# Performance work log

Hardware: AMD Instinct MI355X
Metric: run time of the kernel (lower is better)

The kernel has to match this reference:

```python
import jax, jax.numpy as jnp
import numpy as np

B, L, V, D = 8, 1024, 64, 64  # num_vars == d_model required by the module's g*h broadcast
EPS = 1e-5


def _layer_norm(x, gamma, beta):
    mu = jnp.mean(x, axis=-1, keepdims=True)
    var = jnp.mean(jnp.square(x - mu), axis=-1, keepdims=True)
    return (x - mu) * jax.lax.rsqrt(var + EPS) * gamma + beta


def setup_inputs() -> dict:
    key = jax.random.key(0)
    ks = jax.random.split(key, 20)
    s = 0.05
    inp = {
        'x': jax.random.normal(ks[0], (B, L, V), jnp.float32),
        # per-variable GRN(1, D, D) params, batched over V
        'W1': jax.random.normal(ks[1], (V, D), jnp.float32) * s,   # lin1 weight [in=1 -> D]
        'b1': jax.random.normal(ks[2], (V, D), jnp.float32) * s,
        'W2': jax.random.normal(ks[3], (V, D, D), jnp.float32) * s,
        'b2': jax.random.normal(ks[4], (V, D), jnp.float32) * s,
        'Wg': jax.random.normal(ks[5], (V, D, D), jnp.float32) * s,
        'bg': jax.random.normal(ks[6], (V, D), jnp.float32) * s,
        'Wsk': jax.random.normal(ks[7], (V, D), jnp.float32) * s,  # skip Linear(1, D)
        'bsk': jax.random.normal(ks[8], (V, D), jnp.float32) * s,
        'gamma': jnp.ones((V, D), jnp.float32),
        'beta': jnp.zeros((V, D), jnp.float32),
        # weight_net GRN(V*D, D, V) params
        'Wn1': jax.random.normal(ks[9], (V * D, D), jnp.float32) * s,
        'bn1': jax.random.normal(ks[10], (D,), jnp.float32) * s,
        'Wn2': jax.random.normal(ks[11], (D, D), jnp.float32) * s,
        'bn2': jax.random.normal(ks[12], (D,), jnp.float32) * s,
        'Wng': jax.random.normal(ks[13], (D, V), jnp.float32) * s,
        'bng': jax.random.normal(ks[14], (V,), jnp.float32) * s,
        'Wns': jax.random.normal(ks[15], (V * D, V), jnp.float32) * s,
        'bns': jax.random.normal(ks[16], (V,), jnp.float32) * s,
        'ngamma': jnp.ones((V,), jnp.float32),
        'nbeta': jnp.zeros((V,), jnp.float32),
    }
    return inp


def reference(x, W1, b1, W2, b2, Wg, bg, Wsk, bsk, gamma, beta,
              Wn1, bn1, Wn2, bn2, Wng, bng, Wns, bns, ngamma, nbeta):
    Bx, Lx, Vx = x.shape
    # --- per-variable GRN(1, D, D), batched over the variable axis ---
    h1 = jax.nn.elu(x[..., None] * W1 + b1)                      # [B,L,V,D]
    h2 = jnp.einsum('blvd,vde->blve', h1, W2) + b2               # [B,L,V,D]
    g = jax.nn.sigmoid(jnp.einsum('blvd,vde->blve', h2, Wg) + bg)
    skip = x[..., None] * Wsk + bsk                              # [B,L,V,D]
    stacked = _layer_norm(skip + g * h2, gamma, beta)            # [B,L,V,D]
    # --- weight net GRN(V*D, D, V) + softmax (note: requires V == D) ---
    flat = stacked.reshape(Bx, Lx, Vx * stacked.shape[-1])
    hw = jax.nn.elu(flat @ Wn1 + bn1)                            # [B,L,D]
    hw = hw @ Wn2 + bn2                                          # [B,L,D]
    gw = jax.nn.sigmoid(hw @ Wng + bng)                          # [B,L,V]
    skw = flat @ Wns + bns                                       # [B,L,V]
    weights = jax.nn.softmax(_layer_norm(skw + gw * hw, ngamma, nbeta), axis=-1)
    return jnp.einsum('blv,blvd->bld', weights, stacked)
```

## Files before the change

kernel.cpp:

```cpp
#include <hip/hip_runtime.h>
#include <hip/hip_bf16.h>
#include <math.h>

#define NV 64
#define ND 64
#define NTOK 8192
#define LN_EPS 1e-5f
#define KSPLIT 8
#define KRANGE (4096 / KSPLIT)
#define SROW 4160
#define WROW 4160
#define PROW 1056

typedef __attribute__((ext_vector_type(8))) short s8v;
typedef __attribute__((ext_vector_type(4))) float f4v;
typedef __attribute__((ext_vector_type(4))) int   i4v;

__device__ __forceinline__ float sigm_f(float x) { return 1.f / (1.f + __expf(-x)); }
__device__ __forceinline__ float elu_f(float x)  { return x > 0.f ? x : (__expf(x) - 1.f); }

__device__ __forceinline__ float bf16_to_f(unsigned short s) {
    union { unsigned int u; float f; } c; c.u = ((unsigned int)s) << 16;
    return c.f;
}
__device__ __forceinline__ unsigned short bf16_rn(float f) {
    union { float f; unsigned int u; } c; c.f = f;
    return (unsigned short)((c.u + 0x8000u) >> 16);
}

__global__ __launch_bounds__(256) void vsn_prepack(
    const float* __restrict__ W2, const float* __restrict__ Wg,
    const float* __restrict__ Wn1, const float* __restrict__ Wns,
    short* __restrict__ w2b, short* __restrict__ wgb,
    short* __restrict__ wct)
{
    __shared__ float T[64][65];
    const int b = blockIdx.x, t = threadIdx.x;

    if (b < 64) {
        const float* src = W2 + (size_t)b * 4096;
        short* dst = w2b + (size_t)b * 4096;
        #pragma unroll
        for (int pass = 0; pass < 2; ++pass) {
            #pragma unroll
            for (int i = 0; i < 16; ++i) {
                int id = i * 256 + t;
                T[id & 63][id >> 6] = src[id];
            }
            __syncthreads();
            #pragma unroll
            for (int i = 0; i < 16; ++i) {
                int id = i * 256 + t;
                dst[id] = (short)bf16_rn(T[id >> 6][id & 63]);
            }
            __syncthreads();
            src = Wg + (size_t)b * 4096;
            dst = wgb + (size_t)b * 4096;
        }
    } else {
        int tb = b - 64;
        int half = tb >> 6, kt = tb & 63;
        const float* src = (half == 0 ? Wn1 : Wns) + (size_t)(kt * 64) * 64;
        #pragma unroll
        for (int i = 0; i < 16; ++i) {
            int id = i * 256 + t;
            T[id & 63][id >> 6] = src[id];
        }
        __syncthreads();
        #pragma unroll
        for (int i = 0; i < 16; ++i) {
            int id = i * 256 + t;
            int n = id >> 6, r = id & 63;
            wct[(size_t)(half * 64 + n) * WROW + kt * 64 + r] = (short)bf16_rn(T[n][r]);
        }
    }
}

__global__ __launch_bounds__(256) void vsn_stage1(
    const float* __restrict__ x,
    const float* __restrict__ W1, const float* __restrict__ b1,
    const short* __restrict__ w2b, const short* __restrict__ wgb,
    const float* __restrict__ b2, const float* __restrict__ bg,
    const float* __restrict__ Wsk, const float* __restrict__ bsk,
    const float* __restrict__ gamma, const float* __restrict__ beta,
    unsigned short* __restrict__ stb)
{
    const int t = threadIdx.x;
    const int wave = t >> 6, lane = t & 63;
    const int m16 = lane & 15, quad = lane >> 4;
    const int v = blockIdx.y * 4 + wave;

    __shared__ float xs[4][32];
    __shared__ __align__(16) unsigned short h2s[4][32][72];

    float w1k[2][8], b1k[2][8];
    #pragma unroll
    for (int kt = 0; kt < 2; ++kt) {
        *(float4*)&w1k[kt][0] = *(const float4*)(W1 + v * 64 + kt * 32 + quad * 8);
        *(float4*)&w1k[kt][4] = *(const float4*)(W1 + v * 64 + kt * 32 + quad * 8 + 4);
        *(float4*)&b1k[kt][0] = *(const float4*)(b1 + v * 64 + kt * 32 + quad * 8);
        *(float4*)&b1k[kt][4] = *(const float4*)(b1 + v * 64 + kt * 32 + quad * 8 + 4);
    }
    float b2d[4], bgd[4], wskd[4], bskd[4], gamd[4], betd[4];
    #pragma unroll
    for (int ni = 0; ni < 4; ++ni) {
        int d = v * 64 + ni * 16 + m16;
        b2d[ni] = b2[d]; bgd[ni] = bg[d]; wskd[ni] = Wsk[d]; bskd[ni] = bsk[d];
        gamd[ni] = gamma[d]; betd[ni] = beta[d];
    }
    const size_t wb = (size_t)v * 4096;

    for (int tt4 = 0; tt4 < 4; ++tt4) {
        const int tile0 = blockIdx.x * 128 + tt4 * 32;

        if (lane < 32) xs[wave][lane] = x[(size_t)(tile0 + lane) * NV + v];

        s8v a[2][2];
        #pragma unroll
        for (int kt = 0; kt < 2; ++kt)
            #pragma unroll
            for (int mi = 0; mi < 2; ++mi) {
                float xv = xs[wave][mi * 16 + m16];
                float h[8];
                #pragma unroll
                for (int j = 0; j < 8; ++j) h[j] = elu_f(fmaf(xv, w1k[kt][j], b1k[kt][j]));
                i4v av;
                #pragma unroll
                for (int p = 0; p < 4; ++p) {
                    unsigned int u0 = __float_as_uint(h[2 * p]);
                    unsigned int u1 = __float_as_uint(h[2 * p + 1]);
                    av[p] = (int)((u1 & 0xffff0000u) | (u0 >> 16));
                }
                a[mi][kt] = *(s8v*)&av;
            }

        f4v hacc[2][4];
        #pragma unroll
        for (int mi = 0; mi < 2; ++mi)
            #pragma unroll
            for (int ni = 0; ni < 4; ++ni) hacc[mi][ni] = (f4v){0.f, 0.f, 0.f, 0.f};
        #pragma unroll
        for (int ni = 0; ni < 4; ++ni)
            #pragma unroll
            for (int kt = 0; kt < 2; ++kt) {
                s8v bh = *(const s8v*)(w2b + wb + (size_t)(ni * 16 + m16) * 64 + kt * 32 + quad * 8);
                #pragma unroll
                for (int mi = 0; mi < 2; ++mi)
                    hacc[mi][ni] = __builtin_amdgcn_mfma_f32_16x16x32_bf16(a[mi][kt], bh, hacc[mi][ni], 0, 0, 0);
            }
        #pragma unroll
        for (int mi = 0; mi < 2; ++mi)
            #pragma unroll
            for (int ni = 0; ni < 4; ++ni)
                #pragma unroll
                for (int r = 0; r < 4; ++r) hacc[mi][ni][r] += b2d[ni];

        #pragma unroll
        for (int mi = 0; mi < 2; ++mi)
            #pragma unroll
            for (int ni = 0; ni < 4; ++ni)
                #pragma unroll
                for (int r = 0; r < 4; ++r)
                    h2s[wave][mi * 16 + quad * 4 + r][ni * 16 + m16] =
                        (unsigned short)(__float_as_uint(hacc[mi][ni][r]) >> 16);

        s8v c[2][2];
        #pragma unroll
        for (int mi = 0; mi < 2; ++mi)
            #pragma unroll
            for (int kt = 0; kt < 2; ++kt)
                c[mi][kt] = *(const s8v*)&h2s[wave][mi * 16 + m16][kt * 32 + quad * 8];

        f4v gacc[2][4];
        #pragma unroll
        for (int mi = 0; mi < 2; ++mi)
            #pragma unroll
            for (int ni = 0; ni < 4; ++ni) gacc[mi][ni] = (f4v){0.f, 0.f, 0.f, 0.f};
        #pragma unroll
        for (int ni = 0; ni < 4; ++ni)
            #pragma unroll
            for (int kt = 0; kt < 2; ++kt) {
                s8v bh = *(const s8v*)(wgb + wb + (size_t)(ni * 16 + m16) * 64 + kt * 32 + quad * 8);
                #pragma unroll
                for (int mi = 0; mi < 2; ++mi)
                    gacc[mi][ni] = __builtin_amdgcn_mfma_f32_16x16x32_bf16(c[mi][kt], bh, gacc[mi][ni], 0, 0, 0);
            }

        {
            float xtok[2][4];
            #pragma unroll
            for (int mi = 0; mi < 2; ++mi)
                #pragma unroll
                for (int r = 0; r < 4; ++r) xtok[mi][r] = xs[wave][mi * 16 + quad * 4 + r];
            #pragma unroll
            for (int mi = 0; mi < 2; ++mi)
                #pragma unroll
                for (int ni = 0; ni < 4; ++ni)
                    #pragma unroll
                    for (int r = 0; r < 4; ++r) {
                        float g = sigm_f(gacc[mi][ni][r] + bgd[ni]);
                        gacc[mi][ni][r] = fmaf(xtok[mi][r], wskd[ni], bskd[ni]) + g * hacc[mi][ni][r];
                    }
        }

        #pragma unroll
        for (int mi = 0; mi < 2; ++mi)
            #pragma unroll
            for (int r = 0; r < 4; ++r) {
                float s0 = gacc[mi][0][r], s1 = gacc[mi][1][r], s2 = gacc[mi][2][r], s3 = gacc[mi][3][r];
                float sum = s0 + s1 + s2 + s3;
                float sq  = s0 * s0 + s1 * s1 + s2 * s2 + s3 * s3;
                #pragma unroll
                for (int m = 1; m < 16; m <<= 1) { sum += __shfl_xor(sum, m); sq += __shfl_xor(sq, m); }
                float mu  = sum * 0.015625f;
                float var = sq * 0.015625f - mu * mu;
                float rs  = rsqrtf(var + LN_EPS);
                size_t base = (size_t)(tile0 + mi * 16 + quad * 4 + r) * SROW + (size_t)v * 64 + m16;
                #pragma unroll
                for (int ni = 0; ni < 4; ++ni)
                    stb[base + ni * 16] =
                        bf16_rn((gacc[mi][ni][r] - mu) * rs * gamd[ni] + betd[ni]);
            }
    }
}

__global__ __launch_bounds__(512) void vsn_stage2a(
    const unsigned short* __restrict__ stb,
    const short* __restrict__ wct,
    float* __restrict__ part)
{
    const int t = threadIdx.x;
    const int wave = t >> 6, lane = t & 63;
    const int mtile = wave >> 2;
    const int n0 = (wave & 3) * 32;
    const int tok0 = blockIdx.x * 128 + mtile * 64;
    const int s = blockIdx.y;
    const int k0 = s * KRANGE;
    const int m16 = lane & 15, quad = lane >> 4;

    const short* A = (const short*)stb;

    f4v acc[4][2];
    #pragma unroll
    for (int i = 0; i < 4; ++i)
        #pragma unroll
        for (int j = 0; j < 2; ++j)
            acc[i][j] = (f4v){0.f, 0.f, 0.f, 0.f};

    const short* arow = A   + (size_t)(tok0 + m16) * SROW + quad * 8;
    const short* brow = wct + (size_t)(n0 + m16) * WROW + quad * 8;

    for (int k = k0; k < k0 + KRANGE; k += 32) {
        s8v a[4], b[2];
        #pragma unroll
        for (int i = 0; i < 4; ++i)
            a[i] = *(const s8v*)(arow + (size_t)i * 16 * SROW + k);
        #pragma unroll
        for (int j = 0; j < 2; ++j)
            b[j] = *(const s8v*)(brow + (size_t)j * 16 * WROW + k);
        #pragma unroll
        for (int i = 0; i < 4; ++i)
            #pragma unroll
            for (int j = 0; j < 2; ++j)
                acc[i][j] = __builtin_amdgcn_mfma_f32_16x16x32_bf16(a[i], b[j], acc[i][j], 0, 0, 0);
    }

    #pragma unroll
    for (int i = 0; i < 4; ++i)
        #pragma unroll
        for (int j = 0; j < 2; ++j)
            #pragma unroll
            for (int r = 0; r < 4; ++r)
                part[(size_t)(tok0 + i * 16 + quad * 4 + r) * PROW
                     + s * 128 + n0 + j * 16 + m16] = acc[i][j][r];
}

__global__ __launch_bounds__(256) void vsn_stage2b(
    const unsigned short* __restrict__ stb, const float* __restrict__ part,
    const float* __restrict__ bn1,
    const float* __restrict__ Wn2, const float* __restrict__ bn2,
    const float* __restrict__ Wng, const float* __restrict__ bng,
    const float* __restrict__ bns,
    const float* __restrict__ ngamma, const float* __restrict__ nbeta,
    float* __restrict__ out)
{
    const int t = threadIdx.x;
    const int tok0 = blockIdx.x * 8;
    const int lane = t & 63, wv = t >> 6;

    __shared__ __align__(16) float hw1_s[8][64];
    __shared__ __align__(16) float skw_s[8][64];
    __shared__ __align__(16) float hw2_s[8][64];
    __shared__ float s2_s[8][64];
    __shared__ float w_s[8][64];

    #pragma unroll
    for (int tk = 0; tk < 2; ++tk) {
        int tl = wv * 2 + tk;
        const float* pr = part + (size_t)(tok0 + tl) * PROW
                        + (lane >> 5) * 128 + (lane & 31) * 4;
        float tv[4] = {0.f, 0.f, 0.f, 0.f};
        #pragma unroll
        for (int i = 0; i < 4; ++i) {
            float4 a = *(const float4*)(pr + i * 256);
            tv[0] += a.x; tv[1] += a.y; tv[2] += a.z; tv[3] += a.w;
        }
        #pragma unroll
        for (int c = 0; c < 4; ++c) tv[c] += __shfl_xor(tv[c], 32);
        if (lane < 16) {
            int j0 = lane * 4;
            float4 bb = *(const float4*)(bn1 + j0);
            hw1_s[tl][j0 + 0] = elu_f(tv[0] + bb.x);
            hw1_s[tl][j0 + 1] = elu_f(tv[1] + bb.y);
            hw1_s[tl][j0 + 2] = elu_f(tv[2] + bb.z);
            hw1_s[tl][j0 + 3] = elu_f(tv[3] + bb.w);
        } else if (lane < 32) {
            int j0 = (lane - 16) * 4;
            float4 bb = *(const float4*)(bns + j0);
            skw_s[tl][j0 + 0] = tv[0] + bb.x;
            skw_s[tl][j0 + 1] = tv[1] + bb.y;
            skw_s[tl][j0 + 2] = tv[2] + bb.z;
            skw_s[tl][j0 + 3] = tv[3] + bb.w;
        }
    }
    __syncthreads();

    #pragma unroll
    for (int i = 0; i < 2; ++i) {
        int oidx = i * 256 + t;
        int tt = oidx >> 6, jj = oidx & 63;
        float acc = bn2[jj];
        #pragma unroll
        for (int k4 = 0; k4 < 16; ++k4) {
            float4 h = *(const float4*)&hw1_s[tt][k4 * 4];
            acc += h.x * Wn2[(k4*4+0)*64+jj] + h.y * Wn2[(k4*4+1)*64+jj]
                 + h.z * Wn2[(k4*4+2)*64+jj] + h.w * Wn2[(k4*4+3)*64+jj];
        }
        hw2_s[tt][jj] = acc;
    }
    __syncthreads();

    #pragma unroll
    for (int i = 0; i < 2; ++i) {
        int oidx = i * 256 + t;
        int tt = oidx >> 6, vv = oidx & 63;
        float acc = bng[vv];
        #pragma unroll
        for (int k4 = 0; k4 < 16; ++k4) {
            float4 h = *(const float4*)&hw2_s[tt][k4 * 4];
            acc += h.x * Wng[(k4*4+0)*64+vv] + h.y * Wng[(k4*4+1)*64+vv]
                 + h.z * Wng[(k4*4+2)*64+vv] + h.w * Wng[(k4*4+3)*64+vv];
        }
        float gw = sigm_f(acc);
        s2_s[tt][vv] = skw_s[tt][vv] + gw * hw2_s[tt][vv];
    }
    __syncthreads();

    const int vloc = lane >> 3, d8 = (lane & 7) * 8;
    s8v r0[8], r1[8];
    {
        const short* s0 = (const short*)stb + (size_t)(tok0 + wv * 2) * SROW + d8;
        const short* s1 = s0 + SROW;
        #pragma unroll
        for (int vc = 0; vc < 8; ++vc) {
            r0[vc] = *(const s8v*)(s0 + (vc * 8 + vloc) * 64);
            r1[vc] = *(const s8v*)(s1 + (vc * 8 + vloc) * 64);
        }
    }

    if (t < 128) {
        int tt = t >> 4, l = t & 15;
        float z[4]; float sum = 0.f, sq = 0.f;
        #pragma unroll
        for (int i = 0; i < 4; ++i) { z[i] = s2_s[tt][l + 16 * i]; sum += z[i]; sq += z[i] * z[i]; }
        #pragma unroll
        for (int m = 1; m < 16; m <<= 1) { sum += __shfl_xor(sum, m); sq += __shfl_xor(sq, m); }
        float mu  = sum * 0.015625f;
        float var = sq * 0.015625f - mu * mu;
        float rs  = rsqrtf(var + LN_EPS);
        float ln[4]; float mx = -1e30f;
        #pragma unroll
        for (int i = 0; i < 4; ++i) {
            ln[i] = (z[i] - mu) * rs * ngamma[l + 16 * i] + nbeta[l + 16 * i];
            mx = fmaxf(mx, ln[i]);
        }
        #pragma unroll
        for (int m = 1; m < 16; m <<= 1) mx = fmaxf(mx, __shfl_xor(mx, m));
        float es = 0.f; float ev[4];
        #pragma unroll
        for (int i = 0; i < 4; ++i) { ev[i] = __expf(ln[i] - mx); es += ev[i]; }
        #pragma unroll
        for (int m = 1; m < 16; m <<= 1) es += __shfl_xor(es, m);
        float inv = 1.f / es;
        #pragma unroll
        for (int i = 0; i < 4; ++i) w_s[tt][l + 16 * i] = ev[i] * inv;
    }
    __syncthreads();

    {
        float acc0[8], acc1[8];
        #pragma unroll
        for (int j = 0; j < 8; ++j) { acc0[j] = 0.f; acc1[j] = 0.f; }
        #pragma unroll
        for (int vc = 0; vc < 8; ++vc) {
            int v = vc * 8 + vloc;
            float w0 = w_s[wv * 2][v], w1 = w_s[wv * 2 + 1][v];
            #pragma unroll
            for (int j = 0; j < 8; ++j) {
                acc0[j] = fmaf(w0, bf16_to_f((unsigned short)r0[vc][j]), acc0[j]);
                acc1[j] = fmaf(w1, bf16_to_f((unsigned short)r1[vc][j]), acc1[j]);
            }
        }
        #pragma unroll
        for (int m = 8; m <= 32; m <<= 1)
            #pragma unroll
            for (int j = 0; j < 8; ++j) {
                acc0[j] += __shfl_xor(acc0[j], m);
                acc1[j] += __shfl_xor(acc1[j], m);
            }
        if (lane < 8) {
            float* op = out + (size_t)(tok0 + wv * 2) * 64 + lane * 8;
            *(float4*)op       = make_float4(acc0[0], acc0[1], acc0[2], acc0[3]);
            *(float4*)(op + 4) = make_float4(acc0[4], acc0[5], acc0[6], acc0[7]);
            op += 64;
            *(float4*)op       = make_float4(acc1[0], acc1[1], acc1[2], acc1[3]);
            *(float4*)(op + 4) = make_float4(acc1[4], acc1[5], acc1[6], acc1[7]);
        }
    }
}

extern "C" void kernel_launch(void* const* d_in, const int* in_sizes, int n_in,
                              void* d_out, int out_size, void* d_ws, size_t ws_size,
                              hipStream_t stream) {
    const float* x     = (const float*)d_in[0];
    const float* W1    = (const float*)d_in[1];
    const float* b1    = (const float*)d_in[2];
    const float* W2    = (const float*)d_in[3];
    const float* b2    = (const float*)d_in[4];
    const float* Wg    = (const float*)d_in[5];
    const float* bg    = (const float*)d_in[6];
    const float* Wsk   = (const float*)d_in[7];
    const float* bsk   = (const float*)d_in[8];
    const float* gamma = (const float*)d_in[9];
    const float* beta  = (const float*)d_in[10];
    const float* Wn1   = (const float*)d_in[11];
    const float* bn1   = (const float*)d_in[12];
    const float* Wn2   = (const float*)d_in[13];
    const float* bn2   = (const float*)d_in[14];
    const float* Wng   = (const float*)d_in[15];
    const float* bng   = (const float*)d_in[16];
    const float* Wns   = (const float*)d_in[17];
    const float* bns   = (const float*)d_in[18];
    const float* ngam  = (const float*)d_in[19];
    const float* nbet  = (const float*)d_in[20];

    char* ws = (char*)d_ws;
    unsigned short* stb = (unsigned short*)ws;
    short* wct = (short*)(ws + (70u << 20));
    float* part = (float*)(ws + (72u << 20));
    short* w2b = (short*)(ws + (108u << 20));
    short* wgb = w2b + 262144;
    float* outp = (float*)d_out;

    vsn_prepack<<<dim3(192), 256, 0, stream>>>(W2, Wg, Wn1, Wns, w2b, wgb, wct);
    vsn_stage1<<<dim3(NTOK / 128, 16), 256, 0, stream>>>(
        x, W1, b1, w2b, wgb, b2, bg, Wsk, bsk, gamma, beta, stb);
    vsn_stage2a<<<dim3(NTOK / 128, KSPLIT), 512, 0, stream>>>(stb, wct, part);
    vsn_stage2b<<<dim3(NTOK / 8), 256, 0, stream>>>(
        stb, part, bn1, Wn2, bn2, Wng, bng, bns, ngam, nbet, outp);
}
```

Baseline: 222.8 us.

## Fuse split-K weight-net GEMM into epilogue kernel with in-LDS reduction

Merges the split-K GEMM kernel and the weight-net epilogue kernel into one 1024-thread kernel handling 32 tokens per block. The four K-quarters are reduced through shared memory instead of a global partial-sum buffer. This removes the global write and read of partials and one launch. In exchange, per-block tiles are smaller, so each block rereads the full Wn1/Wns weight matrix for only 32 tokens. The large LDS footprint also limits occupancy.

```diff
diff --git a/kernel.cpp b/kernel.cpp
--- a/kernel.cpp
+++ b/kernel.cpp
@@ -6,11 +6,8 @@
 #define ND 64
 #define NTOK 8192
 #define LN_EPS 1e-5f
-#define KSPLIT 8
-#define KRANGE (4096 / KSPLIT)
 #define SROW 4160
 #define WROW 4160
-#define PROW 1056
 
 typedef __attribute__((ext_vector_type(8))) short s8v;
 typedef __attribute__((ext_vector_type(4))) float f4v;
@@ -224,59 +221,9 @@
     }
 }
 
-__global__ __launch_bounds__(512) void vsn_stage2a(
+__global__ __launch_bounds__(1024) void vsn_stage2(
     const unsigned short* __restrict__ stb,
     const short* __restrict__ wct,
-    float* __restrict__ part)
-{
-    const int t = threadIdx.x;
-    const int wave = t >> 6, lane = t & 63;
-    const int mtile = wave >> 2;
-    const int n0 = (wave & 3) * 32;
-    const int tok0 = blockIdx.x * 128 + mtile * 64;
-    const int s = blockIdx.y;
-    const int k0 = s * KRANGE;
-    const int m16 = lane & 15, quad = lane >> 4;
-
-    const short* A = (const short*)stb;
-
-    f4v acc[4][2];
-    #pragma unroll
-    for (int i = 0; i < 4; ++i)
-        #pragma unroll
-        for (int j = 0; j < 2; ++j)
-            acc[i][j] = (f4v){0.f, 0.f, 0.f, 0.f};
-
-    const short* arow = A   + (size_t)(tok0 + m16) * SROW + quad * 8;
-    const short* brow = wct + (size_t)(n0 + m16) * WROW + quad * 8;
-
-    for (int k = k0; k < k0 + KRANGE; k += 32) {
-        s8v a[4], b[2];
-        #pragma unroll
-        for (int i = 0; i < 4; ++i)
-            a[i] = *(const s8v*)(arow + (size_t)i * 16 * SROW + k);
-        #pragma unroll
-        for (int j = 0; j < 2; ++j)
-            b[j] = *(const s8v*)(brow + (size_t)j * 16 * WROW + k);
-        #pragma unroll
-        for (int i = 0; i < 4; ++i)
-            #pragma unroll
-            for (int j = 0; j < 2; ++j)
-                acc[i][j] = __builtin_amdgcn_mfma_f32_16x16x32_bf16(a[i], b[j], acc[i][j], 0, 0, 0);
-    }
-
-    #pragma unroll
-    for (int i = 0; i < 4; ++i)
-        #pragma unroll
-        for (int j = 0; j < 2; ++j)
-            #pragma unroll
-            for (int r = 0; r < 4; ++r)
-                part[(size_t)(tok0 + i * 16 + quad * 4 + r) * PROW
-                     + s * 128 + n0 + j * 16 + m16] = acc[i][j][r];
-}
-
-__global__ __launch_bounds__(256) void vsn_stage2b(
-    const unsigned short* __restrict__ stb, const float* __restrict__ part,
     const float* __restrict__ bn1,
     const float* __restrict__ Wn2, const float* __restrict__ bn2,
     const float* __restrict__ Wng, const float* __restrict__ bng,
@@ -285,81 +232,107 @@
     float* __restrict__ out)
 {
     const int t = threadIdx.x;
-    const int tok0 = blockIdx.x * 8;
-    const int lane = t & 63, wv = t >> 6;
-
-    __shared__ __align__(16) float hw1_s[8][64];
-    __shared__ __align__(16) float skw_s[8][64];
-    __shared__ __align__(16) float hw2_s[8][64];
-    __shared__ float s2_s[8][64];
-    __shared__ float w_s[8][64];
-
-    #pragma unroll
-    for (int tk = 0; tk < 2; ++tk) {
-        int tl = wv * 2 + tk;
-        const float* pr = part + (size_t)(tok0 + tl) * PROW
-                        + (lane >> 5) * 128 + (lane & 31) * 4;
-        float tv[4] = {0.f, 0.f, 0.f, 0.f};
-        #pragma unroll
-        for (int i = 0; i < 4; ++i) {
-            float4 a = *(const float4*)(pr + i * 256);
-            tv[0] += a.x; tv[1] += a.y; tv[2] += a.z; tv[3] += a.w;
-        }
-        #pragma unroll
-        for (int c = 0; c < 4; ++c) tv[c] += __shfl_xor(tv[c], 32);
-        if (lane < 16) {
-            int j0 = lane * 4;
-            float4 bb = *(const float4*)(bn1 + j0);
-            hw1_s[tl][j0 + 0] = elu_f(tv[0] + bb.x);
-            hw1_s[tl][j0 + 1] = elu_f(tv[1] + bb.y);
-            hw1_s[tl][j0 + 2] = elu_f(tv[2] + bb.z);
-            hw1_s[tl][j0 + 3] = elu_f(tv[3] + bb.w);
-        } else if (lane < 32) {
-            int j0 = (lane - 16) * 4;
-            float4 bb = *(const float4*)(bns + j0);
-            skw_s[tl][j0 + 0] = tv[0] + bb.x;
-            skw_s[tl][j0 + 1] = tv[1] + bb.y;
-            skw_s[tl][j0 + 2] = tv[2] + bb.z;
-            skw_s[tl][j0 + 3] = tv[3] + bb.w;
-        }
+    const int wave = t >> 6, lane = t & 63;
+    const int m16 = lane & 15, quad = lane >> 4;
+    const int kq = wave >> 2;
+    const int mtile = wave & 1, nh = (wave >> 1) & 1;
+    const int tok0 = blockIdx.x * 32;
+
+    __shared__ __align__(16) float P[3][32][132];
+    float (*S)[132] = P[0];
+    float* base1 = &P[1][0][0];
+    float (*hw1)[64] = (float(*)[64])base1;
+    float (*skw)[64] = (float(*)[64])(base1 + 2048);
+    float (*hw2)[64] = (float(*)[64])(&P[2][0][0]);
+    float (*s2m)[64] = hw1;
+    float (*wgt)[64] = skw;
+
+    const short* A = (const short*)stb;
+    const int k0 = kq * 1024;
+
+    f4v acc[4];
+    #pragma unroll
+    for (int nj = 0; nj < 4; ++nj) acc[nj] = (f4v){0.f, 0.f, 0.f, 0.f};
+
+    const short* arow = A + (size_t)(tok0 + mtile * 16 + m16) * SROW + k0 + quad * 8;
+    const short* brow = wct + (size_t)(nh * 64 + m16) * WROW + k0 + quad * 8;
+
+    #pragma unroll 4
+    for (int kk = 0; kk < 1024; kk += 32) {
+        s8v a0 = *(const s8v*)(arow + kk);
+        s8v b[4];
+        #pragma unroll
+        for (int nj = 0; nj < 4; ++nj)
+            b[nj] = *(const s8v*)(brow + (size_t)nj * 16 * WROW + kk);
+        #pragma unroll
+        for (int nj = 0; nj < 4; ++nj)
+            acc[nj] = __builtin_amdgcn_mfma_f32_16x16x32_bf16(a0, b[nj], acc[nj], 0, 0, 0);
+    }
+
+    if (kq >= 1) {
+        #pragma unroll
+        for (int nj = 0; nj < 4; ++nj)
+            #pragma unroll
+            for (int r = 0; r < 4; ++r)
+                P[kq - 1][mtile * 16 + quad * 4 + r][nh * 64 + nj * 16 + m16] = acc[nj][r];
+    }
+    __syncthreads();
+    if (kq == 0) {
+        #pragma unroll
+        for (int nj = 0; nj < 4; ++nj)
+            #pragma unroll
+            for (int r = 0; r < 4; ++r) {
+                int row = mtile * 16 + quad * 4 + r, col = nh * 64 + nj * 16 + m16;
+                float v = acc[nj][r] + P[0][row][col] + P[1][row][col] + P[2][row][col];
+                S[row][col] = v;
+            }
     }
     __syncthreads();
 
     #pragma unroll
     for (int i = 0; i < 2; ++i) {
-        int oidx = i * 256 + t;
-        int tt = oidx >> 6, jj = oidx & 63;
-        float acc = bn2[jj];
+        int idx = i * 1024 + t;
+        int m = idx >> 6, j = idx & 63;
+        hw1[m][j] = elu_f(S[m][j] + bn1[j]);
+        skw[m][j] = S[m][64 + j] + bns[j];
+    }
+    __syncthreads();
+
+    #pragma unroll
+    for (int i = 0; i < 2; ++i) {
+        int idx = i * 1024 + t;
+        int m = idx >> 6, j = idx & 63;
+        float a2 = bn2[j];
         #pragma unroll
         for (int k4 = 0; k4 < 16; ++k4) {
-            float4 h = *(const float4*)&hw1_s[tt][k4 * 4];
-            acc += h.x * Wn2[(k4*4+0)*64+jj] + h.y * Wn2[(k4*4+1)*64+jj]
-                 + h.z * Wn2[(k4*4+2)*64+jj] + h.w * Wn2[(k4*4+3)*64+jj];
-        }
-        hw2_s[tt][jj] = acc;
+            float4 h = *(const float4*)&hw1[m][k4 * 4];
+            a2 += h.x * Wn2[(k4*4+0)*64+j] + h.y * Wn2[(k4*4+1)*64+j]
+                + h.z * Wn2[(k4*4+2)*64+j] + h.w * Wn2[(k4*4+3)*64+j];
+        }
+        hw2[m][j] = a2;
     }
     __syncthreads();
 
     #pragma unroll
     for (int i = 0; i < 2; ++i) {
-        int oidx = i * 256 + t;
-        int tt = oidx >> 6, vv = oidx & 63;
-        float acc = bng[vv];
+        int idx = i * 1024 + t;
+        int m = idx >> 6, vv = idx & 63;
+        float a3 = bng[vv];
         #pragma unroll
         for (int k4 = 0; k4 < 16; ++k4) {
-            float4 h = *(const float4*)&hw2_s[tt][k4 * 4];
-            acc += h.x * Wng[(k4*4+0)*64+vv] + h.y * Wng[(k4*4+1)*64+vv]
-                 + h.z * Wng[(k4*4+2)*64+vv] + h.w * Wng[(k4*4+3)*64+vv];
-        }
-        float gw = sigm_f(acc);
-        s2_s[tt][vv] = skw_s[tt][vv] + gw * hw2_s[tt][vv];
+            float4 h = *(const float4*)&hw2[m][k4 * 4];
+            a3 += h.x * Wng[(k4*4+0)*64+vv] + h.y * Wng[(k4*4+1)*64+vv]
+                + h.z * Wng[(k4*4+2)*64+vv] + h.w * Wng[(k4*4+3)*64+vv];
+        }
+        float gw = sigm_f(a3);
+        s2m[m][vv] = skw[m][vv] + gw * hw2[m][vv];
     }
     __syncthreads();
 
     const int vloc = lane >> 3, d8 = (lane & 7) * 8;
     s8v r0[8], r1[8];
     {
-        const short* s0 = (const short*)stb + (size_t)(tok0 + wv * 2) * SROW + d8;
+        const short* s0 = A + (size_t)(tok0 + wave * 2) * SROW + d8;
         const short* s1 = s0 + SROW;
         #pragma unroll
         for (int vc = 0; vc < 8; ++vc) {
@@ -368,11 +341,11 @@
         }
     }
 
-    if (t < 128) {
+    if (t < 512) {
         int tt = t >> 4, l = t & 15;
         float z[4]; float sum = 0.f, sq = 0.f;
         #pragma unroll
-        for (int i = 0; i < 4; ++i) { z[i] = s2_s[tt][l + 16 * i]; sum += z[i]; sq += z[i] * z[i]; }
+        for (int i = 0; i < 4; ++i) { z[i] = s2m[tt][l + 16 * i]; sum += z[i]; sq += z[i] * z[i]; }
         #pragma unroll
         for (int m = 1; m < 16; m <<= 1) { sum += __shfl_xor(sum, m); sq += __shfl_xor(sq, m); }
         float mu  = sum * 0.015625f;
@@ -393,7 +366,7 @@
         for (int m = 1; m < 16; m <<= 1) es += __shfl_xor(es, m);
         float inv = 1.f / es;
         #pragma unroll
-        for (int i = 0; i < 4; ++i) w_s[tt][l + 16 * i] = ev[i] * inv;
+        for (int i = 0; i < 4; ++i) wgt[tt][l + 16 * i] = ev[i] * inv;
     }
     __syncthreads();
 
@@ -404,7 +377,7 @@
         #pragma unroll
         for (int vc = 0; vc < 8; ++vc) {
             int v = vc * 8 + vloc;
-            float w0 = w_s[wv * 2][v], w1 = w_s[wv * 2 + 1][v];
+            float w0 = wgt[wave * 2][v], w1 = wgt[wave * 2 + 1][v];
             #pragma unroll
             for (int j = 0; j < 8; ++j) {
                 acc0[j] = fmaf(w0, bf16_to_f((unsigned short)r0[vc][j]), acc0[j]);
@@ -419,7 +392,7 @@
                 acc1[j] += __shfl_xor(acc1[j], m);
             }
         if (lane < 8) {
-            float* op = out + (size_t)(tok0 + wv * 2) * 64 + lane * 8;
+            float* op = out + (size_t)(tok0 + wave * 2) * 64 + lane * 8;
             *(float4*)op       = make_float4(acc0[0], acc0[1], acc0[2], acc0[3]);
             *(float4*)(op + 4) = make_float4(acc0[4], acc0[5], acc0[6], acc0[7]);
             op += 64;
@@ -457,15 +430,13 @@
     char* ws = (char*)d_ws;
     unsigned short* stb = (unsigned short*)ws;
     short* wct = (short*)(ws + (70u << 20));
-    float* part = (float*)(ws + (72u << 20));
-    short* w2b = (short*)(ws + (108u << 20));
+    short* w2b = (short*)(ws + (72u << 20));
     short* wgb = w2b + 262144;
     float* outp = (float*)d_out;
 
     vsn_prepack<<<dim3(192), 256, 0, stream>>>(W2, Wg, Wn1, Wns, w2b, wgb, wct);
     vsn_stage1<<<dim3(NTOK / 128, 16), 256, 0, stream>>>(
         x, W1, b1, w2b, wgb, b2, bg, Wsk, bsk, gamma, beta, stb);
-    vsn_stage2a<<<dim3(NTOK / 128, KSPLIT), 512, 0, stream>>>(stb, wct, part);
-    vsn_stage2b<<<dim3(NTOK / 8), 256, 0, stream>>>(
-        stb, part, bn1, Wn2, bn2, Wng, bng, bns, ngam, nbet, outp);
-}
+    vsn_stage2<<<dim3(NTOK / 32), 1024, 0, stream>>>(
+        stb, wct, bn1, Wn2, bn2, Wng, bng, bns, ngam, nbet, outp);
+}
```

After: 240.6 us. 1.08x slower.

## Stage weight-net GEMM tiles through LDS with register prefetch and finer K-split

Applied to the files above, without the earlier changes.

Rewrites the split-K GEMM of flattened stacked activations against the weight-net matrices so each 256-thread block stages 128x64 bf16 tiles of A and B into padded shared memory. It prefetches the next K chunk into registers while computing on the current one. Each wave now computes a 32x128 output tile, so B fragments are reused from LDS instead of being reloaded from global memory. The K split doubles to 16, which doubles the partial-sum buffer that stage2b must reduce. Row strides drop their padding (4160 to 4096), which may reintroduce cache-set conflicts on global loads, and the workspace layout is compacted.

```diff
diff --git a/kernel.cpp b/kernel.cpp
--- a/kernel.cpp
+++ b/kernel.cpp
@@ -6,11 +6,12 @@
 #define ND 64
 #define NTOK 8192
 #define LN_EPS 1e-5f
-#define KSPLIT 8
-#define KRANGE (4096 / KSPLIT)
-#define SROW 4160
-#define WROW 4160
-#define PROW 1056
+#define SROW 4096
+#define WROW 4096
+#define KSPLIT 16
+#define KR2 (4096 / KSPLIT)
+#define BK 64
+#define PROW2 (KSPLIT * 128)
 
 typedef __attribute__((ext_vector_type(8))) short s8v;
 typedef __attribute__((ext_vector_type(4))) float f4v;
@@ -224,55 +225,81 @@
     }
 }
 
-__global__ __launch_bounds__(512) void vsn_stage2a(
+__global__ __launch_bounds__(256) void vsn_stage2a(
     const unsigned short* __restrict__ stb,
     const short* __restrict__ wct,
     float* __restrict__ part)
 {
     const int t = threadIdx.x;
     const int wave = t >> 6, lane = t & 63;
-    const int mtile = wave >> 2;
-    const int n0 = (wave & 3) * 32;
-    const int tok0 = blockIdx.x * 128 + mtile * 64;
+    const int m16 = lane & 15, quad = lane >> 4;
+    const int tok0 = blockIdx.x * 128;
     const int s = blockIdx.y;
-    const int k0 = s * KRANGE;
-    const int m16 = lane & 15, quad = lane >> 4;
-
+    const int k0 = s * KR2;
+
+    __shared__ __align__(16) unsigned short Al[128][72];
+    __shared__ __align__(16) unsigned short Bl[128][72];
+
+    const int srow = t >> 3;
+    const int scol = (t & 7) * 8;
     const short* A = (const short*)stb;
 
-    f4v acc[4][2];
-    #pragma unroll
-    for (int i = 0; i < 4; ++i)
-        #pragma unroll
-        for (int j = 0; j < 2; ++j)
-            acc[i][j] = (f4v){0.f, 0.f, 0.f, 0.f};
-
-    const short* arow = A   + (size_t)(tok0 + m16) * SROW + quad * 8;
-    const short* brow = wct + (size_t)(n0 + m16) * WROW + quad * 8;
-
-    for (int k = k0; k < k0 + KRANGE; k += 32) {
-        s8v a[4], b[2];
-        #pragma unroll
-        for (int i = 0; i < 4; ++i)
-            a[i] = *(const s8v*)(arow + (size_t)i * 16 * SROW + k);
-        #pragma unroll
-        for (int j = 0; j < 2; ++j)
-            b[j] = *(const s8v*)(brow + (size_t)j * 16 * WROW + k);
-        #pragma unroll
-        for (int i = 0; i < 4; ++i)
-            #pragma unroll
-            for (int j = 0; j < 2; ++j)
-                acc[i][j] = __builtin_amdgcn_mfma_f32_16x16x32_bf16(a[i], b[j], acc[i][j], 0, 0, 0);
-    }
-
-    #pragma unroll
-    for (int i = 0; i < 4; ++i)
-        #pragma unroll
-        for (int j = 0; j < 2; ++j)
+    f4v acc[2][8];
+    #pragma unroll
+    for (int mi = 0; mi < 2; ++mi)
+        #pragma unroll
+        for (int nj = 0; nj < 8; ++nj) acc[mi][nj] = (f4v){0.f, 0.f, 0.f, 0.f};
+
+    s8v pa[4], pb[4];
+    #pragma unroll
+    for (int q = 0; q < 4; ++q) {
+        int row = srow + q * 32;
+        pa[q] = *(const s8v*)(A + (size_t)(tok0 + row) * SROW + k0 + scol);
+        pb[q] = *(const s8v*)(wct + (size_t)row * WROW + k0 + scol);
+    }
+
+    for (int kc = 0; kc < KR2 / BK; ++kc) {
+        if (kc > 0) __syncthreads();
+        #pragma unroll
+        for (int q = 0; q < 4; ++q) {
+            int row = srow + q * 32;
+            *(s8v*)&Al[row][scol] = pa[q];
+            *(s8v*)&Bl[row][scol] = pb[q];
+        }
+        __syncthreads();
+        if (kc + 1 < KR2 / BK) {
+            int kn = k0 + (kc + 1) * BK;
+            #pragma unroll
+            for (int q = 0; q < 4; ++q) {
+                int row = srow + q * 32;
+                pa[q] = *(const s8v*)(A + (size_t)(tok0 + row) * SROW + kn + scol);
+                pb[q] = *(const s8v*)(wct + (size_t)row * WROW + kn + scol);
+            }
+        }
+        #pragma unroll
+        for (int ks = 0; ks < 2; ++ks) {
+            s8v af[2], bf[8];
+            af[0] = *(const s8v*)&Al[wave * 32 + m16][ks * 32 + quad * 8];
+            af[1] = *(const s8v*)&Al[wave * 32 + 16 + m16][ks * 32 + quad * 8];
+            #pragma unroll
+            for (int nj = 0; nj < 8; ++nj)
+                bf[nj] = *(const s8v*)&Bl[nj * 16 + m16][ks * 32 + quad * 8];
+            #pragma unroll
+            for (int nj = 0; nj < 8; ++nj) {
+                acc[0][nj] = __builtin_amdgcn_mfma_f32_16x16x32_bf16(af[0], bf[nj], acc[0][nj], 0, 0, 0);
+                acc[1][nj] = __builtin_amdgcn_mfma_f32_16x16x32_bf16(af[1], bf[nj], acc[1][nj], 0, 0, 0);
+            }
+        }
+    }
+
+    #pragma unroll
+    for (int mi = 0; mi < 2; ++mi)
+        #pragma unroll
+        for (int nj = 0; nj < 8; ++nj)
             #pragma unroll
             for (int r = 0; r < 4; ++r)
-                part[(size_t)(tok0 + i * 16 + quad * 4 + r) * PROW
-                     + s * 128 + n0 + j * 16 + m16] = acc[i][j][r];
+                part[(size_t)(tok0 + wave * 32 + mi * 16 + quad * 4 + r) * PROW2
+                     + s * 128 + nj * 16 + m16] = acc[mi][nj][r];
 }
 
 __global__ __launch_bounds__(256) void vsn_stage2b(
@@ -297,11 +324,11 @@
     #pragma unroll
     for (int tk = 0; tk < 2; ++tk) {
         int tl = wv * 2 + tk;
-        const float* pr = part + (size_t)(tok0 + tl) * PROW
+        const float* pr = part + (size_t)(tok0 + tl) * PROW2
                         + (lane >> 5) * 128 + (lane & 31) * 4;
         float tv[4] = {0.f, 0.f, 0.f, 0.f};
         #pragma unroll
-        for (int i = 0; i < 4; ++i) {
+        for (int i = 0; i < 8; ++i) {
             float4 a = *(const float4*)(pr + i * 256);
             tv[0] += a.x; tv[1] += a.y; tv[2] += a.z; tv[3] += a.w;
         }
@@ -456,16 +483,16 @@
 
     char* ws = (char*)d_ws;
     unsigned short* stb = (unsigned short*)ws;
-    short* wct = (short*)(ws + (70u << 20));
-    float* part = (float*)(ws + (72u << 20));
-    short* w2b = (short*)(ws + (108u << 20));
+    short* wct = (short*)(ws + (64u << 20));
+    short* w2b = (short*)(ws + (65u << 20));
     short* wgb = w2b + 262144;
+    float* part = (float*)(ws + (66u << 20));
     float* outp = (float*)d_out;
 
     vsn_prepack<<<dim3(192), 256, 0, stream>>>(W2, Wg, Wn1, Wns, w2b, wgb, wct);
     vsn_stage1<<<dim3(NTOK / 128, 16), 256, 0, stream>>>(
         x, W1, b1, w2b, wgb, b2, bg, Wsk, bsk, gamma, beta, stb);
-    vsn_stage2a<<<dim3(NTOK / 128, KSPLIT), 512, 0, stream>>>(stb, wct, part);
+    vsn_stage2a<<<dim3(NTOK / 128, KSPLIT), 256, 0, stream>>>(stb, wct, part);
     vsn_stage2b<<<dim3(NTOK / 8), 256, 0, stream>>>(
         stb, part, bn1, Wn2, bn2, Wng, bng, bns, ngam, nbet, outp);
 }
```

Result: faster. 202.0 us (-9.3%).
